# Kernel optimization log

Measured on AMD Instinct MI355X. Metric: run time of the kernel, lower is better.

## Reference

```python
import jax, jax.numpy as jnp
import numpy as np

B, C, H, W = 2048, 16, 32, 32
F = C * H * W  # 16384, flattened feature dim
NAN_FRAC = 0.1


def setup_inputs() -> dict:
    key = jax.random.key(0)
    k1, k2, k3, k4, k5, k6 = jax.random.split(key, 6)
    output = jax.random.normal(k1, (B, C, H, W), dtype=jnp.float32)
    target = jax.random.normal(k2, (B, C, H, W), dtype=jnp.float32)
    # inject NaNs so the nan-omission path is exercised
    nan_mask = jax.random.uniform(k6, (B, C, H, W)) < NAN_FRAC
    target = jnp.where(nan_mask, jnp.nan, target)
    e_exp = jax.random.uniform(k3, (B, 1), dtype=jnp.float32)
    sample_weight = jax.random.uniform(k4, (B, 1), dtype=jnp.float32)
    feature_weight = jax.random.uniform(k5, (F, 1), dtype=jnp.float32)
    return {"output": output, "target": target, "e_exp": e_exp,
            "sample_weight": sample_weight, "feature_weight": feature_weight}


def reference(output, target, e_exp, sample_weight, feature_weight):
    # NaN-omitted, feature-weighted, per-sample-normalized MSE.
    # (e_exp and sample_weight are accepted but unused, as in the original.)
    num_pos = ~jnp.isnan(target)                       # [B,C,H,W] bool
    tgt = jnp.where(num_pos, target, 0.0)
    maskf = num_pos.astype(output.dtype)
    residual = (tgt - output) * maskf                  # [B,C,H,W]
    residual = residual.reshape(residual.shape[0], -1)  # [B,F]
    # torch.mm(residual, diag(fw)) == residual * fw^T (elementwise, same math)
    standardized = residual * feature_weight[:, 0][None, :]  # [B,F]
    per_sample = jnp.sum(standardized ** 2, axis=1) / jnp.sum(
        maskf.reshape(maskf.shape[0], -1), axis=1)     # [B]
    return jnp.sum(per_sample)
```

## Files before the change

kernel.cpp:

```cpp
#include <hip/hip_runtime.h>
#include <math.h>


#define B_SAMPLES 2048
#define F_FEATURES 16384
#define THREADS 256
#define VEC_PER_THREAD (F_FEATURES / 4 / THREADS)

__global__ __launch_bounds__(THREADS) void fnmse_kernel(
    const float* __restrict__ output,
    const float* __restrict__ target,
    const float* __restrict__ fw,
    float* __restrict__ out)
{
    const int b = blockIdx.x;
    const int tid = threadIdx.x;

    const float4* __restrict__ out4 = (const float4*)(output + (size_t)b * F_FEATURES);
    const float4* __restrict__ tgt4 = (const float4*)(target + (size_t)b * F_FEATURES);
    const float4* __restrict__ fw4  = (const float4*)fw;

    float sumsq = 0.0f;
    float cnt   = 0.0f;

    #pragma unroll
    for (int i = 0; i < VEC_PER_THREAD; ++i) {
        const int v = i * THREADS + tid;
        float4 o = out4[v];
        float4 t = tgt4[v];
        float4 w = fw4[v];

        {
            const bool m = !isnan(t.x);
            const float r = m ? (t.x - o.x) * w.x : 0.0f;
            sumsq = fmaf(r, r, sumsq);
            cnt += m ? 1.0f : 0.0f;
        }
        {
            const bool m = !isnan(t.y);
            const float r = m ? (t.y - o.y) * w.y : 0.0f;
            sumsq = fmaf(r, r, sumsq);
            cnt += m ? 1.0f : 0.0f;
        }
        {
            const bool m = !isnan(t.z);
            const float r = m ? (t.z - o.z) * w.z : 0.0f;
            sumsq = fmaf(r, r, sumsq);
            cnt += m ? 1.0f : 0.0f;
        }
        {
            const bool m = !isnan(t.w);
            const float r = m ? (t.w - o.w) * w.w : 0.0f;
            sumsq = fmaf(r, r, sumsq);
            cnt += m ? 1.0f : 0.0f;
        }
    }

    #pragma unroll
    for (int off = 32; off > 0; off >>= 1) {
        sumsq += __shfl_down(sumsq, off, 64);
        cnt   += __shfl_down(cnt,   off, 64);
    }

    __shared__ float s_sq[THREADS / 64];
    __shared__ float s_ct[THREADS / 64];
    const int wave = tid >> 6;
    const int lane = tid & 63;
    if (lane == 0) { s_sq[wave] = sumsq; s_ct[wave] = cnt; }
    __syncthreads();

    if (tid == 0) {
        float sq = s_sq[0] + s_sq[1] + s_sq[2] + s_sq[3];
        float ct = s_ct[0] + s_ct[1] + s_ct[2] + s_ct[3];
        atomicAdd(out, sq / ct);
    }
}

extern "C" void kernel_launch(void* const* d_in, const int* in_sizes, int n_in,
                              void* d_out, int out_size, void* d_ws, size_t ws_size,
                              hipStream_t stream) {
    const float* output = (const float*)d_in[0];
    const float* target = (const float*)d_in[1];
    const float* fw     = (const float*)d_in[4];
    float* out = (float*)d_out;

    hipMemsetAsync(out, 0, sizeof(float), stream);

    fnmse_kernel<<<B_SAMPLES, THREADS, 0, stream>>>(output, target, fw, out);
}
```

Before: 281.5 us.

## Split each sample across four blocks and add a separate finalize kernel

Result: faster. 273.6 us (-2.8%).

```diff
diff --git a/kernel.cpp b/kernel.cpp
--- a/kernel.cpp
+++ b/kernel.cpp
@@ -5,54 +5,57 @@
 #define B_SAMPLES 2048
 #define F_FEATURES 16384
 #define THREADS 256
-#define VEC_PER_THREAD (F_FEATURES / 4 / THREADS)
+#define CHUNKS 4
+#define F_CHUNK (F_FEATURES / CHUNKS)
+#define V_PER_THREAD (F_CHUNK / 4 / THREADS)
 
-__global__ __launch_bounds__(THREADS) void fnmse_kernel(
+__global__ __launch_bounds__(THREADS) void fnmse_partial(
     const float* __restrict__ output,
     const float* __restrict__ target,
     const float* __restrict__ fw,
-    float* __restrict__ out)
+    float* __restrict__ ws_sq,
+    float* __restrict__ ws_ct)
 {
-    const int b = blockIdx.x;
+    const int b = blockIdx.x >> 2;
+    const int c = blockIdx.x & 3;
     const int tid = threadIdx.x;
 
-    const float4* __restrict__ out4 = (const float4*)(output + (size_t)b * F_FEATURES);
-    const float4* __restrict__ tgt4 = (const float4*)(target + (size_t)b * F_FEATURES);
-    const float4* __restrict__ fw4  = (const float4*)fw;
+    const float4* __restrict__ o4 = (const float4*)(output + (size_t)b * F_FEATURES + c * F_CHUNK);
+    const float4* __restrict__ t4 = (const float4*)(target + (size_t)b * F_FEATURES + c * F_CHUNK);
+    const float4* __restrict__ w4 = (const float4*)(fw + c * F_CHUNK);
+
+    float4 o[V_PER_THREAD], t[V_PER_THREAD], w[V_PER_THREAD];
+    #pragma unroll
+    for (int k = 0; k < V_PER_THREAD; ++k) {
+        const int v = k * THREADS + tid;
+        o[k] = o4[v];
+        t[k] = t4[v];
+        w[k] = w4[v];
+    }
 
     float sumsq = 0.0f;
     float cnt   = 0.0f;
-
     #pragma unroll
-    for (int i = 0; i < VEC_PER_THREAD; ++i) {
-        const int v = i * THREADS + tid;
-        float4 o = out4[v];
-        float4 t = tgt4[v];
-        float4 w = fw4[v];
-
+    for (int k = 0; k < V_PER_THREAD; ++k) {
         {
-            const bool m = !isnan(t.x);
-            const float r = m ? (t.x - o.x) * w.x : 0.0f;
-            sumsq = fmaf(r, r, sumsq);
-            cnt += m ? 1.0f : 0.0f;
+            const bool m = !isnan(t[k].x);
+            const float r = m ? (t[k].x - o[k].x) * w[k].x : 0.0f;
+            sumsq = fmaf(r, r, sumsq); cnt += m ? 1.0f : 0.0f;
         }
         {
-            const bool m = !isnan(t.y);
-            const float r = m ? (t.y - o.y) * w.y : 0.0f;
-            sumsq = fmaf(r, r, sumsq);
-            cnt += m ? 1.0f : 0.0f;
+            const bool m = !isnan(t[k].y);
+            const float r = m ? (t[k].y - o[k].y) * w[k].y : 0.0f;
+            sumsq = fmaf(r, r, sumsq); cnt += m ? 1.0f : 0.0f;
         }
         {
-            const bool m = !isnan(t.z);
-            const float r = m ? (t.z - o.z) * w.z : 0.0f;
-            sumsq = fmaf(r, r, sumsq);
-            cnt += m ? 1.0f : 0.0f;
+            const bool m = !isnan(t[k].z);
+            const float r = m ? (t[k].z - o[k].z) * w[k].z : 0.0f;
+            sumsq = fmaf(r, r, sumsq); cnt += m ? 1.0f : 0.0f;
         }
         {
-            const bool m = !isnan(t.w);
-            const float r = m ? (t.w - o.w) * w.w : 0.0f;
-            sumsq = fmaf(r, r, sumsq);
-            cnt += m ? 1.0f : 0.0f;
+            const bool m = !isnan(t[k].w);
+            const float r = m ? (t[k].w - o[k].w) * w[k].w : 0.0f;
+            sumsq = fmaf(r, r, sumsq); cnt += m ? 1.0f : 0.0f;
         }
     }
 
@@ -70,10 +73,35 @@
     __syncthreads();
 
     if (tid == 0) {
-        float sq = s_sq[0] + s_sq[1] + s_sq[2] + s_sq[3];
-        float ct = s_ct[0] + s_ct[1] + s_ct[2] + s_ct[3];
-        atomicAdd(out, sq / ct);
+        const float sq = s_sq[0] + s_sq[1] + s_sq[2] + s_sq[3];
+        const float ct = s_ct[0] + s_ct[1] + s_ct[2] + s_ct[3];
+        atomicAdd(&ws_sq[b], sq);
+        atomicAdd(&ws_ct[b], ct);
     }
+}
+
+__global__ __launch_bounds__(THREADS) void fnmse_finalize(
+    const float* __restrict__ ws_sq,
+    const float* __restrict__ ws_ct,
+    float* __restrict__ out)
+{
+    const int tid = threadIdx.x;
+    float acc = 0.0f;
+    #pragma unroll
+    for (int s = 0; s < B_SAMPLES / THREADS; ++s) {
+        const int b = s * THREADS + tid;
+        acc += ws_sq[b] / ws_ct[b];
+    }
+    #pragma unroll
+    for (int off = 32; off > 0; off >>= 1)
+        acc += __shfl_down(acc, off, 64);
+
+    __shared__ float s_a[THREADS / 64];
+    const int wave = tid >> 6;
+    const int lane = tid & 63;
+    if (lane == 0) s_a[wave] = acc;
+    __syncthreads();
+    if (tid == 0) out[0] = s_a[0] + s_a[1] + s_a[2] + s_a[3];
 }
 
 extern "C" void kernel_launch(void* const* d_in, const int* in_sizes, int n_in,
@@ -84,7 +112,11 @@
     const float* fw     = (const float*)d_in[4];
     float* out = (float*)d_out;
 
-    hipMemsetAsync(out, 0, sizeof(float), stream);
+    float* ws_sq = (float*)d_ws;
+    float* ws_ct = ws_sq + B_SAMPLES;
 
-    fnmse_kernel<<<B_SAMPLES, THREADS, 0, stream>>>(output, target, fw, out);
+    hipMemsetAsync(d_ws, 0, 2 * B_SAMPLES * sizeof(float), stream);
+
+    fnmse_partial<<<B_SAMPLES * CHUNKS, THREADS, 0, stream>>>(output, target, fw, ws_sq, ws_ct);
+    fnmse_finalize<<<1, THREADS, 0, stream>>>(ws_sq, ws_ct, out);
 }
```
